# Performance work log

Measured on AMD Instinct MI355X. Metric: run time of the kernel, lower is better.

## Reference

```python
import jax, jax.numpy as jnp
import numpy as np

N = 100000
E = 1600000
IN_CH = 32
HID = 64
HEADS = 2
NUM_CLASSES = 12
NEG_SLOPE = 0.2


def gat_conv(x, src, dst, W, a_src, a_dst, bias, concat):
    """PyG-style GATConv (self-loops already appended to src/dst).
    x: [N, F_in], W: [F_in, H*C], a_src/a_dst: [H, C], bias: [H*C] or [C]."""
    n = x.shape[0]
    h = (x @ W).reshape(n, HEADS, -1)                    # [N, H, C]
    al_s = jnp.einsum('nhc,hc->nh', h, a_src)            # [N, H]
    al_d = jnp.einsum('nhc,hc->nh', h, a_dst)            # [N, H]
    e = jax.nn.leaky_relu(al_s[src] + al_d[dst], NEG_SLOPE)  # [Etot, H]
    # segment softmax over destination neighborhoods
    e_max = jax.ops.segment_max(e, dst, num_segments=n)      # [N, H]
    ex = jnp.exp(e - e_max[dst])                              # [Etot, H]
    denom = jax.ops.segment_sum(ex, dst, num_segments=n)     # [N, H]
    alpha = ex / denom[dst]                                   # [Etot, H]
    msg = h[src] * alpha[:, :, None]                          # [Etot, H, C]
    out = jax.ops.segment_sum(msg, dst, num_segments=n)      # [N, H, C]
    if concat:
        out = out.reshape(n, -1)
    else:
        out = out.mean(axis=1)
    return out + bias


def prelu(x, a):
    return jnp.where(x >= 0, x, a * x)


def setup_inputs() -> dict:
    key = jax.random.key(0)
    ks = jax.random.split(key, 16)
    HC = HEADS * HID
    d = {
        'x': jax.random.normal(ks[0], (N, IN_CH), jnp.float32),
        'edge_index': jax.random.randint(ks[1], (2, E), 0, N, jnp.int32),
        'W1': jax.random.normal(ks[2], (IN_CH, HC), jnp.float32) * 0.1,
        'a1s': jax.random.normal(ks[3], (HEADS, HID), jnp.float32) * 0.1,
        'a1d': jax.random.normal(ks[4], (HEADS, HID), jnp.float32) * 0.1,
        'b1': jnp.zeros((HC,), jnp.float32),
        'W2': jax.random.normal(ks[5], (HC, HC), jnp.float32) * 0.1,
        'a2s': jax.random.normal(ks[6], (HEADS, HID), jnp.float32) * 0.1,
        'a2d': jax.random.normal(ks[7], (HEADS, HID), jnp.float32) * 0.1,
        'b2': jnp.zeros((HC,), jnp.float32),
        'W3': jax.random.normal(ks[8], (HC, HC), jnp.float32) * 0.1,
        'a3s': jax.random.normal(ks[9], (HEADS, HID), jnp.float32) * 0.1,
        'a3d': jax.random.normal(ks[10], (HEADS, HID), jnp.float32) * 0.1,
        'b3': jnp.zeros((HID,), jnp.float32),
        'prelu_a': jnp.float32(0.25),
        'Wc': jax.random.normal(ks[11], (HID, NUM_CLASSES), jnp.float32) * 0.1,
        'bc': jnp.zeros((NUM_CLASSES,), jnp.float32),
    }
    return d


def reference(x, edge_index, W1, a1s, a1d, b1, W2, a2s, a2d, b2,
              W3, a3s, a3d, b3, prelu_a, Wc, bc):
    loops = jnp.arange(N, dtype=edge_index.dtype)
    src = jnp.concatenate([edge_index[0], loops])
    dst = jnp.concatenate([edge_index[1], loops])
    h = gat_conv(x, src, dst, W1, a1s, a1d, b1, concat=True)
    h = prelu(h, prelu_a)
    h = gat_conv(h, src, dst, W2, a2s, a2d, b2, concat=True)
    h = prelu(h, prelu_a)
    h = gat_conv(h, src, dst, W3, a3s, a3d, b3, concat=False)
    h = prelu(h, prelu_a)
    return h @ Wc + bc
```

## Files before the change

### kernel.cpp

```cpp
#include <hip/hip_runtime.h>
#include <stdint.h>

#define NN 100000
#define NE 1600000
#define ET (NE + NN)
#define HC 128
#define HID 64
#define NCLS 12
#define BSZ 512
#define NBK ((NN + BSZ - 1) / BSZ)
#define CHUNK 8192
#define NPB ((ET + CHUNK - 1) / CHUNK)

typedef _Float16 f16;
typedef _Float16 f16x2 __attribute__((ext_vector_type(2)));
typedef _Float16 f16x4 __attribute__((ext_vector_type(4)));
typedef _Float16 f16x8 __attribute__((ext_vector_type(8)));

__global__ void k_init(int* bucketTotal) {
    int i = threadIdx.x;
    if (i < NBK) bucketTotal[i] = 0;
}

__global__ __launch_bounds__(256) void k_hist(const int* __restrict__ ei, int* __restrict__ bucketTotal) {
    __shared__ int h[NBK];
    int tid = threadIdx.x;
    for (int b = tid; b < NBK; b += 256) h[b] = 0;
    __syncthreads();
    long base = (long)blockIdx.x * CHUNK;
#pragma unroll
    for (int k = 0; k < CHUNK / 256; k++) {
        long i = base + k * 256 + tid;
        if (i < ET) {
            int d = (i < NE) ? ei[NE + i] : (int)(i - NE);
            atomicAdd(&h[d >> 9], 1);
        }
    }
    __syncthreads();
    for (int b = tid; b < NBK; b += 256)
        if (h[b]) atomicAdd(&bucketTotal[b], h[b]);
}

__global__ __launch_bounds__(256) void k_bscan(const int* __restrict__ bucketTotal,
                                               int* __restrict__ bucketStart,
                                               int* __restrict__ bucketFill,
                                               int* __restrict__ rp) {
    __shared__ int s[256];
    int tid = threadIdx.x;
    int v = (tid < NBK) ? bucketTotal[tid] : 0;
    s[tid] = v;
    __syncthreads();
    for (int o = 1; o < 256; o <<= 1) {
        int t = (tid >= o) ? s[tid - o] : 0;
        __syncthreads();
        s[tid] += t;
        __syncthreads();
    }
    if (tid < NBK) {
        int excl = s[tid] - v;
        bucketStart[tid] = excl;
        bucketFill[tid] = excl;
    }
    if (tid == 0) { bucketStart[NBK] = ET; rp[NN] = ET; }
}

__global__ __launch_bounds__(256) void k_part(const int* __restrict__ ei,
                                              int* __restrict__ bucketFill,
                                              uint32_t* __restrict__ ebuf) {
    __shared__ int h[NBK];
    __shared__ int base[NBK];
    int tid = threadIdx.x;
    for (int b = tid; b < NBK; b += 256) h[b] = 0;
    __syncthreads();
    long cbase = (long)blockIdx.x * CHUNK;
#pragma unroll
    for (int k = 0; k < CHUNK / 256; k++) {
        long i = cbase + k * 256 + tid;
        if (i < ET) {
            int d = (i < NE) ? ei[NE + i] : (int)(i - NE);
            atomicAdd(&h[d >> 9], 1);
        }
    }
    __syncthreads();
    for (int b = tid; b < NBK; b += 256)
        base[b] = h[b] ? atomicAdd(&bucketFill[b], h[b]) : 0;
    __syncthreads();
    for (int b = tid; b < NBK; b += 256) h[b] = 0;
    __syncthreads();
#pragma unroll
    for (int k = 0; k < CHUNK / 256; k++) {
        long i = cbase + k * 256 + tid;
        if (i < ET) {
            int s, d;
            if (i < NE) { s = ei[i]; d = ei[NE + i]; } else { s = d = (int)(i - NE); }
            int bk = d >> 9;
            int off = atomicAdd(&h[bk], 1);
            ebuf[base[bk] + off] = (uint32_t)s | ((uint32_t)(d & 511) << 17);
        }
    }
}

__global__ __launch_bounds__(512) void k_build(const uint32_t* __restrict__ ebuf,
                                               const int* __restrict__ bucketStart,
                                               int* __restrict__ rp, int* __restrict__ colx) {
    __shared__ int cnt[BSZ];
    __shared__ int fill[BSZ];
    int b = blockIdx.x, tid = threadIdx.x;
    int e0 = bucketStart[b], e1 = bucketStart[b + 1], m = e1 - e0;
    cnt[tid] = 0;
    __syncthreads();
    for (int k = tid; k < m; k += 512) atomicAdd(&cnt[ebuf[e0 + k] >> 17], 1);
    __syncthreads();
    int v = cnt[tid];
    __syncthreads();
    cnt[tid] = v;
    __syncthreads();
    for (int o = 1; o < 512; o <<= 1) {
        int t = (tid >= o) ? cnt[tid - o] : 0;
        __syncthreads();
        cnt[tid] += t;
        __syncthreads();
    }
    int excl = cnt[tid] - v;
    int node = b * BSZ + tid;
    if (node < NN) rp[node] = e0 + excl;
    fill[tid] = e0 + excl;
    __syncthreads();
    for (int k = tid; k < m; k += 512) {
        uint32_t e = ebuf[e0 + k];
        int pos = atomicAdd(&fill[e >> 17], 1);
        colx[pos] = (int)(e & 0x1FFFF);
    }
}

__global__ __launch_bounds__(256) void k_att1(const float* __restrict__ x,
                                              const float* __restrict__ W1,
                                              const float* __restrict__ a1s,
                                              const float* __restrict__ a1d,
                                              f16* __restrict__ x16,
                                              float* __restrict__ als, float* __restrict__ ald) {
    __shared__ float sIn[128 * 33];
    __shared__ float spv[128];
    int t = threadIdx.x;
    long n0 = (long)blockIdx.x * 128;
    if (t < 128) {
        int sd = t >> 6, h = (t >> 5) & 1, f = t & 31;
        const float* a = sd ? a1d : a1s;
        float acc = 0.f;
        for (int c = 0; c < 64; c++) acc = fmaf(W1[f * HC + h * 64 + c], a[h * 64 + c], acc);
        spv[t] = acc;
    }
    for (int c = t; c < 128 * 8; c += 256) {
        int row = c >> 3, col = (c & 7) * 4;
        long gn = n0 + row;
        if (gn < NN) {
            float4 v = *(const float4*)(x + gn * 32 + col);
            float* dst = &sIn[row * 33 + col];
            dst[0] = v.x; dst[1] = v.y; dst[2] = v.z; dst[3] = v.w;
            f16x4 o;
            o[0] = (f16)v.x; o[1] = (f16)v.y; o[2] = (f16)v.z; o[3] = (f16)v.w;
            *(f16x4*)(x16 + gn * 32 + col) = o;
        }
    }
    __syncthreads();
    int n = t >> 1, h = t & 1;
    long gn = n0 + n;
    if (gn >= NN) return;
    const float* row = &sIn[n * 33];
    const float* as_ = &spv[h * 32];
    const float* ad_ = &spv[64 + h * 32];
    float s_ = 0.f, d_ = 0.f;
#pragma unroll
    for (int f = 0; f < 32; f++) {
        float v = row[f];
        s_ = fmaf(v, as_[f], s_);
        d_ = fmaf(v, ad_[f], d_);
    }
    als[2 * gn + h] = s_;
    ald[2 * gn + h] = d_;
}

__global__ __launch_bounds__(256) void k_aggx(const int* __restrict__ rp, const int* __restrict__ colx,
                                              const f16* __restrict__ x16,
                                              const float* __restrict__ als, const float* __restrict__ ald,
                                              float* __restrict__ xbar) {
    int wid = blockIdx.x * 4 + (threadIdx.x >> 6);
    int lane = threadIdx.x & 63;
    int g = lane >> 2, li = lane & 3;
    int start = rp[wid], end = rp[wid + 1];
    float2 adv = *(const float2*)(ald + 2 * wid);
    float a0[8], a1[8];
#pragma unroll
    for (int k = 0; k < 8; k++) { a0[k] = 0.f; a1[k] = 0.f; }
    float ws0 = 0.f, ws1 = 0.f;
#pragma unroll 2
    for (int j0 = start; j0 < end; j0 += 16) {
        int j = j0 + g;
        int jc = j < end ? j : end - 1;
        int s = colx[jc];
        float2 asv = *(const float2*)(als + 2 * s);
        float e0 = asv.x + adv.x, e1 = asv.y + adv.y;
        e0 = fmaxf(e0, 0.2f * e0);
        e1 = fmaxf(e1, 0.2f * e1);
        float w0 = __expf(e0), w1 = __expf(e1);
        if (j >= end) { w0 = 0.f; w1 = 0.f; }
        ws0 += w0; ws1 += w1;
        f16x8 xv = *(const f16x8*)(x16 + (long)s * 32 + li * 8);
#pragma unroll
        for (int k = 0; k < 8; k++) {
            float f = (float)xv[k];
            a0[k] = fmaf(w0, f, a0[k]);
            a1[k] = fmaf(w1, f, a1[k]);
        }
    }
#pragma unroll
    for (int o = 4; o <= 32; o <<= 1) {
        ws0 += __shfl_xor(ws0, o);
        ws1 += __shfl_xor(ws1, o);
#pragma unroll
        for (int k = 0; k < 8; k++) {
            a0[k] += __shfl_xor(a0[k], o);
            a1[k] += __shfl_xor(a1[k], o);
        }
    }
    float inv0 = 1.0f / ws0, inv1 = 1.0f / ws1;
    int head = g >> 3, q = g & 7;
    float val = head ? a1[q] * inv1 : a0[q] * inv0;
    xbar[(long)wid * 64 + head * 32 + li * 8 + q] = val;
}

__global__ __launch_bounds__(256) void k_post1(const float* __restrict__ xb,
                                               const float* __restrict__ W1,
                                               const float* __restrict__ b1,
                                               const float* __restrict__ pap,
                                               float* __restrict__ outp) {
    __shared__ __align__(16) float sIn[64 * 64];
    __shared__ __align__(16) float sW[32 * HC];
    __shared__ float sB[HC];
    int tid = threadIdx.x;
    long n0 = (long)blockIdx.x * 64;
    for (int c = tid; c < 64 * 16; c += 256) {
        int row = c >> 4, col = (c & 15) * 4;
        long gn = n0 + row;
        float4 v = make_float4(0.f, 0.f, 0.f, 0.f);
        if (gn < NN) v = *(const float4*)(xb + gn * 64 + col);
        *(float4*)(sIn + row * 64 + col) = v;
    }
    for (int c = tid; c < 32 * HC / 4; c += 256) ((float4*)sW)[c] = ((const float4*)W1)[c];
    if (tid < HC) sB[tid] = b1[tid];
    __syncthreads();
    int cg = tid & 31, ng = tid >> 5, head = cg >> 4;
    float4 acc[8];
#pragma unroll
    for (int i = 0; i < 8; i++) acc[i] = make_float4(0.f, 0.f, 0.f, 0.f);
    for (int k = 0; k < 32; k++) {
        float4 w = *(const float4*)(sW + k * HC + cg * 4);
#pragma unroll
        for (int i = 0; i < 8; i++) {
            float a = sIn[(ng * 8 + i) * 64 + head * 32 + k];
            acc[i].x = fmaf(a, w.x, acc[i].x);
            acc[i].y = fmaf(a, w.y, acc[i].y);
            acc[i].z = fmaf(a, w.z, acc[i].z);
            acc[i].w = fmaf(a, w.w, acc[i].w);
        }
    }
    float pa = pap[0];
    float4 b = *(const float4*)(sB + cg * 4);
#pragma unroll
    for (int i = 0; i < 8; i++) {
        long n = n0 + ng * 8 + i;
        if (n < NN) {
            float4 o;
            o.x = acc[i].x + b.x; o.y = acc[i].y + b.y;
            o.z = acc[i].z + b.z; o.w = acc[i].w + b.w;
            o.x = o.x >= 0.f ? o.x : pa * o.x;
            o.y = o.y >= 0.f ? o.y : pa * o.y;
            o.z = o.z >= 0.f ? o.z : pa * o.z;
            o.w = o.w >= 0.f ? o.w : pa * o.w;
            *(float4*)(outp + n * HC + cg * 4) = o;
        }
    }
}

__global__ __launch_bounds__(256) void k_gemm(const float* __restrict__ xg,
                                              const float* __restrict__ Wg,
                                              const float* __restrict__ avs,
                                              const float* __restrict__ avd,
                                              f16* __restrict__ h16,
                                              float* __restrict__ als, float* __restrict__ ald) {
    constexpr int K = 128, KT = 64;
    __shared__ __align__(16) float sIn[64 * KT];
    __shared__ __align__(16) float sW[KT * HC];
    __shared__ float sas[HC], sad[HC];
    int tid = threadIdx.x;
    long n0 = (long)blockIdx.x * 64;
    if (tid < HC) { sas[tid] = avs[tid]; sad[tid] = avd[tid]; }
    int cg = tid & 31, ng = tid >> 5;
    float4 acc[8];
#pragma unroll
    for (int i = 0; i < 8; i++) acc[i] = make_float4(0.f, 0.f, 0.f, 0.f);

    for (int kt = 0; kt < K; kt += KT) {
        __syncthreads();
        const float4* wsrc = (const float4*)(Wg + (long)kt * HC);
        for (int c = tid; c < KT * HC / 4; c += 256) ((float4*)sW)[c] = wsrc[c];
        for (int c = tid; c < 64 * KT / 4; c += 256) {
            int row = c / (KT / 4), kc = c % (KT / 4);
            long gn = n0 + row;
            float4 v = make_float4(0.f, 0.f, 0.f, 0.f);
            if (gn < NN) v = *(const float4*)(xg + gn * K + kt + kc * 4);
            *(float4*)(sIn + row * KT + kc * 4) = v;
        }
        __syncthreads();
        for (int k = 0; k < KT; k += 4) {
            float4 w0 = *(const float4*)(sW + (k + 0) * HC + cg * 4);
            float4 w1 = *(const float4*)(sW + (k + 1) * HC + cg * 4);
            float4 w2 = *(const float4*)(sW + (k + 2) * HC + cg * 4);
            float4 w3 = *(const float4*)(sW + (k + 3) * HC + cg * 4);
#pragma unroll
            for (int i = 0; i < 8; i++) {
                float4 a = *(const float4*)(sIn + (ng * 8 + i) * KT + k);
                acc[i].x = fmaf(a.x, w0.x, acc[i].x); acc[i].y = fmaf(a.x, w0.y, acc[i].y);
                acc[i].z = fmaf(a.x, w0.z, acc[i].z); acc[i].w = fmaf(a.x, w0.w, acc[i].w);
                acc[i].x = fmaf(a.y, w1.x, acc[i].x); acc[i].y = fmaf(a.y, w1.y, acc[i].y);
                acc[i].z = fmaf(a.y, w1.z, acc[i].z); acc[i].w = fmaf(a.y, w1.w, acc[i].w);
                acc[i].x = fmaf(a.z, w2.x, acc[i].x); acc[i].y = fmaf(a.z, w2.y, acc[i].y);
                acc[i].z = fmaf(a.z, w2.z, acc[i].z); acc[i].w = fmaf(a.z, w2.w, acc[i].w);
                acc[i].x = fmaf(a.w, w3.x, acc[i].x); acc[i].y = fmaf(a.w, w3.y, acc[i].y);
                acc[i].z = fmaf(a.w, w3.z, acc[i].z); acc[i].w = fmaf(a.w, w3.w, acc[i].w);
            }
        }
    }
    int head = cg >> 4;
#pragma unroll
    for (int i = 0; i < 8; i++) {
        long n = n0 + ng * 8 + i;
        if (n < NN) {
            f16x4 o;
            o[0] = (f16)acc[i].x; o[1] = (f16)acc[i].y;
            o[2] = (f16)acc[i].z; o[3] = (f16)acc[i].w;
            *(f16x4*)(h16 + n * HC + cg * 4) = o;
        }
        const float* ap = (const float*)&acc[i];
        float s_ = 0.f, d_ = 0.f;
#pragma unroll
        for (int j = 0; j < 4; j++) {
            int c = cg * 4 + j;
            s_ = fmaf(ap[j], sas[c], s_);
            d_ = fmaf(ap[j], sad[c], d_);
        }
#pragma unroll
        for (int o = 8; o; o >>= 1) { s_ += __shfl_xor(s_, o); d_ += __shfl_xor(d_, o); }
        if ((cg & 15) == 0 && n < NN) {
            als[2 * n + head] = s_;
            ald[2 * n + head] = d_;
        }
    }
}

template <int MEAN>
__global__ __launch_bounds__(256) void k_agg(const int* __restrict__ rp, const int* __restrict__ colx,
                                             const f16* __restrict__ h,
                                             const float* __restrict__ als, const float* __restrict__ ald,
                                             const float* __restrict__ bias,
                                             const float* __restrict__ pap,
                                             float* __restrict__ outp) {
    int wid = blockIdx.x * 4 + (threadIdx.x >> 6);
    int lane = threadIdx.x & 63;
    int g = lane >> 4, li = lane & 15;
    int start = rp[wid], end = rp[wid + 1];
    float2 adv = *(const float2*)(ald + 2 * wid);
    float acc[8];
#pragma unroll
    for (int k = 0; k < 8; k++) acc[k] = 0.f;
    float ws0 = 0.f, ws1 = 0.f;
    bool head1 = li >= 8;
#pragma unroll 4
    for (int j0 = start; j0 < end; j0 += 4) {
        int j = j0 + g;
        int jc = j < end ? j : end - 1;
        int s = colx[jc];
        float2 asv = *(const float2*)(als + 2 * s);
        float e0 = asv.x + adv.x, e1 = asv.y + adv.y;
        e0 = fmaxf(e0, 0.2f * e0);
        e1 = fmaxf(e1, 0.2f * e1);
        float w0 = __expf(e0), w1 = __expf(e1);
        if (j >= end) { w0 = 0.f; w1 = 0.f; }
        ws0 += w0; ws1 += w1;
        f16x8 hv = *(const f16x8*)(h + (long)s * HC + li * 8);
        float wsel = head1 ? w1 : w0;
#pragma unroll
        for (int k = 0; k < 8; k++) acc[k] = fmaf(wsel, (float)hv[k], acc[k]);
    }
#pragma unroll
    for (int o = 16; o <= 32; o <<= 1) {
        ws0 += __shfl_xor(ws0, o);
        ws1 += __shfl_xor(ws1, o);
#pragma unroll
        for (int k = 0; k < 8; k++) acc[k] += __shfl_xor(acc[k], o);
    }
    float pa = pap[0];
    if (!MEAN) {
        float inv = 1.0f / (head1 ? ws1 : ws0);
        int c = li * 8 + g * 2;
        float2 bu = *(const float2*)(bias + c);
        float o0 = acc[g * 2] * inv + bu.x;
        float o1 = acc[g * 2 + 1] * inv + bu.y;
        o0 = o0 >= 0.f ? o0 : pa * o0;
        o1 = o1 >= 0.f ? o1 : pa * o1;
        *(float2*)(outp + (long)wid * HC + c) = make_float2(o0, o1);
    } else {
        float inv = 1.0f / (head1 ? ws1 : ws0);
        float v0 = acc[g * 2] * inv, v1 = acc[g * 2 + 1] * inv;
        float p0 = __shfl_xor(v0, 8), p1 = __shfl_xor(v1, 8);
        if (!head1) {
            int c = li * 8 + g * 2;
            float2 bu = *(const float2*)(bias + c);
            float o0 = 0.5f * (v0 + p0) + bu.x;
            float o1 = 0.5f * (v1 + p1) + bu.y;
            o0 = o0 >= 0.f ? o0 : pa * o0;
            o1 = o1 >= 0.f ? o1 : pa * o1;
            *(float2*)(outp + (long)wid * HID + c) = make_float2(o0, o1);
        }
    }
}

__global__ __launch_bounds__(256) void k_cls(const float* __restrict__ hin,
                                             const float* __restrict__ Wc,
                                             const float* __restrict__ bcp,
                                             float* __restrict__ outp) {
    __shared__ float sW[HID * NCLS];
    __shared__ float sb[NCLS];
    int tid = threadIdx.x;
    for (int c = tid; c < HID * NCLS; c += 256) sW[c] = Wc[c];
    if (tid < NCLS) sb[tid] = bcp[tid];
    __syncthreads();
    int n = blockIdx.x * 256 + tid;
    if (n >= NN) return;
    float o[NCLS];
#pragma unroll
    for (int k = 0; k < NCLS; k++) o[k] = sb[k];
    const float* row = hin + (long)n * HID;
#pragma unroll 8
    for (int c = 0; c < HID; c++) {
        float v = row[c];
#pragma unroll
        for (int k = 0; k < NCLS; k++) o[k] = fmaf(v, sW[c * NCLS + k], o[k]);
    }
#pragma unroll
    for (int k = 0; k < NCLS; k += 2)
        *(float2*)(outp + (long)n * NCLS + k) = make_float2(o[k], o[k + 1]);
}

extern "C" void kernel_launch(void* const* d_in, const int* in_sizes, int n_in,
                              void* d_out, int out_size, void* d_ws, size_t ws_size,
                              hipStream_t stream) {
    const float* x   = (const float*)d_in[0];
    const int*   ei  = (const int*)d_in[1];
    const float* W1  = (const float*)d_in[2];
    const float* a1s = (const float*)d_in[3];
    const float* a1d = (const float*)d_in[4];
    const float* b1  = (const float*)d_in[5];
    const float* W2  = (const float*)d_in[6];
    const float* a2s = (const float*)d_in[7];
    const float* a2d = (const float*)d_in[8];
    const float* b2  = (const float*)d_in[9];
    const float* W3  = (const float*)d_in[10];
    const float* a3s = (const float*)d_in[11];
    const float* a3d = (const float*)d_in[12];
    const float* b3  = (const float*)d_in[13];
    const float* pa  = (const float*)d_in[14];
    const float* Wc  = (const float*)d_in[15];
    const float* bc  = (const float*)d_in[16];
    float* out = (float*)d_out;

    char* w = (char*)d_ws;
    size_t off = 0;
    auto take = [&](size_t b) { void* p = w + off; off += (b + 255) & ~(size_t)255; return p; };
    int* rp      = (int*)take((size_t)(NN + 1) * 4);
    int* colx    = (int*)take((size_t)ET * 4);
    int* btot    = (int*)take((size_t)NBK * 4);
    int* bstart  = (int*)take((size_t)(NBK + 1) * 4);
    int* bfill   = (int*)take((size_t)NBK * 4);
    float* als   = (float*)take((size_t)NN * 8);
    float* ald   = (float*)take((size_t)NN * 8);
    f16* x16     = (f16*)take((size_t)NN * 32 * 2);
    f16* h16     = (f16*)take((size_t)NN * HC * 2);
    float* xbar  = (float*)take((size_t)NN * 64 * 4);
    float* bufB  = (float*)take((size_t)NN * HC * 4);
    uint32_t* ebuf = (uint32_t*)h16;

    int nb = (NN + 255) / 256;
    int gb = (NN + 63) / 64;
    int ab = NN / 4;
    int tb = (NN + 127) / 128;

    k_init<<<1, 256, 0, stream>>>(btot);
    k_hist<<<NPB, 256, 0, stream>>>(ei, btot);
    k_bscan<<<1, 256, 0, stream>>>(btot, bstart, bfill, rp);
    k_part<<<NPB, 256, 0, stream>>>(ei, bfill, ebuf);
    k_build<<<NBK, 512, 0, stream>>>(ebuf, bstart, rp, colx);

    k_att1<<<tb, 256, 0, stream>>>(x, W1, a1s, a1d, x16, als, ald);
    k_aggx<<<ab, 256, 0, stream>>>(rp, colx, x16, als, ald, xbar);
    k_post1<<<gb, 256, 0, stream>>>(xbar, W1, b1, pa, bufB);
    k_gemm<<<gb, 256, 0, stream>>>(bufB, W2, a2s, a2d, h16, als, ald);
    k_agg<0><<<ab, 256, 0, stream>>>(rp, colx, h16, als, ald, b2, pa, bufB);
    k_gemm<<<gb, 256, 0, stream>>>(bufB, W3, a3s, a3d, h16, als, ald);
    k_agg<1><<<ab, 256, 0, stream>>>(rp, colx, h16, als, ald, b3, pa, bufB);
    k_cls<<<nb, 256, 0, stream>>>(bufB, Wc, bc, out);
}
```

Before: 524.1 us.

## Use MFMA fp16 GEMM with hi/lo split weights and fp16 intermediate activations

Replaces the fp32 FMA GEMMs for layers 2 and 3 with MFMA 16x16x32 fp16 instructions. The weights are pre-split into hi and lo fp16 fragments to keep accuracy, and a new kernel lays them out in MFMA fragment order. Post-layer activations are now stored in fp16 instead of fp32, which halves GEMM input traffic, and the aggx kernel is reworked to use 16 lanes per feature with 4 edges in flight. This risks some precision loss, since the activations are rounded to fp16.

```diff
diff --git a/kernel.cpp b/kernel.cpp
--- a/kernel.cpp
+++ b/kernel.cpp
@@ -16,6 +16,7 @@
 typedef _Float16 f16x2 __attribute__((ext_vector_type(2)));
 typedef _Float16 f16x4 __attribute__((ext_vector_type(4)));
 typedef _Float16 f16x8 __attribute__((ext_vector_type(8)));
+typedef float f32x4 __attribute__((ext_vector_type(4)));
 
 __global__ void k_init(int* bucketTotal) {
     int i = threadIdx.x;
@@ -130,6 +131,27 @@
         uint32_t e = ebuf[e0 + k];
         int pos = atomicAdd(&fill[e >> 17], 1);
         colx[pos] = (int)(e & 0x1FFFF);
+    }
+}
+
+__global__ void k_wt(const float* __restrict__ W2, const float* __restrict__ W3,
+                     f16* __restrict__ wout) {
+    const float* W = blockIdx.x ? W3 : W2;
+    f16* hi = wout + (size_t)blockIdx.x * 2 * 2048 * 8;
+    f16* lo = hi + 2048 * 8;
+    for (int s = threadIdx.x; s < 2048; s += 256) {
+        int kk = s >> 9, nt = (s >> 6) & 7, l = s & 63;
+        int n = nt * 16 + (l & 15), k0 = kk * 32 + (l >> 4) * 8;
+        f16x8 vh, vl;
+#pragma unroll
+        for (int j = 0; j < 8; j++) {
+            float v = W[(long)(k0 + j) * HC + n];
+            f16 h = (f16)v;
+            vh[j] = h;
+            vl[j] = (f16)(v - (float)h);
+        }
+        *(f16x8*)(hi + (size_t)s * 8) = vh;
+        *(f16x8*)(lo + (size_t)s * 8) = vl;
     }
 }
 
@@ -186,15 +208,12 @@
                                               float* __restrict__ xbar) {
     int wid = blockIdx.x * 4 + (threadIdx.x >> 6);
     int lane = threadIdx.x & 63;
-    int g = lane >> 2, li = lane & 3;
+    int g = lane >> 4, li = lane & 15;
     int start = rp[wid], end = rp[wid + 1];
     float2 adv = *(const float2*)(ald + 2 * wid);
-    float a0[8], a1[8];
-#pragma unroll
-    for (int k = 0; k < 8; k++) { a0[k] = 0.f; a1[k] = 0.f; }
-    float ws0 = 0.f, ws1 = 0.f;
-#pragma unroll 2
-    for (int j0 = start; j0 < end; j0 += 16) {
+    float a00 = 0.f, a01 = 0.f, a10 = 0.f, a11 = 0.f, ws0 = 0.f, ws1 = 0.f;
+#pragma unroll 4
+    for (int j0 = start; j0 < end; j0 += 4) {
         int j = j0 + g;
         int jc = j < end ? j : end - 1;
         int s = colx[jc];
@@ -205,35 +224,31 @@
         float w0 = __expf(e0), w1 = __expf(e1);
         if (j >= end) { w0 = 0.f; w1 = 0.f; }
         ws0 += w0; ws1 += w1;
-        f16x8 xv = *(const f16x8*)(x16 + (long)s * 32 + li * 8);
-#pragma unroll
-        for (int k = 0; k < 8; k++) {
-            float f = (float)xv[k];
-            a0[k] = fmaf(w0, f, a0[k]);
-            a1[k] = fmaf(w1, f, a1[k]);
-        }
-    }
-#pragma unroll
-    for (int o = 4; o <= 32; o <<= 1) {
-        ws0 += __shfl_xor(ws0, o);
-        ws1 += __shfl_xor(ws1, o);
-#pragma unroll
-        for (int k = 0; k < 8; k++) {
-            a0[k] += __shfl_xor(a0[k], o);
-            a1[k] += __shfl_xor(a1[k], o);
-        }
-    }
-    float inv0 = 1.0f / ws0, inv1 = 1.0f / ws1;
-    int head = g >> 3, q = g & 7;
-    float val = head ? a1[q] * inv1 : a0[q] * inv0;
-    xbar[(long)wid * 64 + head * 32 + li * 8 + q] = val;
+        f16x2 xv = *(const f16x2*)(x16 + (long)s * 32 + li * 2);
+        float f0 = (float)xv[0], f1 = (float)xv[1];
+        a00 = fmaf(w0, f0, a00); a01 = fmaf(w0, f1, a01);
+        a10 = fmaf(w1, f0, a10); a11 = fmaf(w1, f1, a11);
+    }
+#pragma unroll
+    for (int o = 16; o <= 32; o <<= 1) {
+        ws0 += __shfl_xor(ws0, o); ws1 += __shfl_xor(ws1, o);
+        a00 += __shfl_xor(a00, o); a01 += __shfl_xor(a01, o);
+        a10 += __shfl_xor(a10, o); a11 += __shfl_xor(a11, o);
+    }
+    if (g == 0) {
+        float inv = 1.0f / ws0;
+        *(float2*)(xbar + (long)wid * 64 + li * 2) = make_float2(a00 * inv, a01 * inv);
+    } else if (g == 1) {
+        float inv = 1.0f / ws1;
+        *(float2*)(xbar + (long)wid * 64 + 32 + li * 2) = make_float2(a10 * inv, a11 * inv);
+    }
 }
 
 __global__ __launch_bounds__(256) void k_post1(const float* __restrict__ xb,
                                                const float* __restrict__ W1,
                                                const float* __restrict__ b1,
                                                const float* __restrict__ pap,
-                                               float* __restrict__ outp) {
+                                               f16* __restrict__ outp) {
     __shared__ __align__(16) float sIn[64 * 64];
     __shared__ __align__(16) float sW[32 * HC];
     __shared__ float sB[HC];
@@ -270,90 +285,76 @@
     for (int i = 0; i < 8; i++) {
         long n = n0 + ng * 8 + i;
         if (n < NN) {
-            float4 o;
-            o.x = acc[i].x + b.x; o.y = acc[i].y + b.y;
-            o.z = acc[i].z + b.z; o.w = acc[i].w + b.w;
-            o.x = o.x >= 0.f ? o.x : pa * o.x;
-            o.y = o.y >= 0.f ? o.y : pa * o.y;
-            o.z = o.z >= 0.f ? o.z : pa * o.z;
-            o.w = o.w >= 0.f ? o.w : pa * o.w;
-            *(float4*)(outp + n * HC + cg * 4) = o;
-        }
-    }
-}
-
-__global__ __launch_bounds__(256) void k_gemm(const float* __restrict__ xg,
-                                              const float* __restrict__ Wg,
-                                              const float* __restrict__ avs,
-                                              const float* __restrict__ avd,
-                                              f16* __restrict__ h16,
-                                              float* __restrict__ als, float* __restrict__ ald) {
-    constexpr int K = 128, KT = 64;
-    __shared__ __align__(16) float sIn[64 * KT];
-    __shared__ __align__(16) float sW[KT * HC];
-    __shared__ float sas[HC], sad[HC];
+            float o0 = acc[i].x + b.x, o1 = acc[i].y + b.y;
+            float o2 = acc[i].z + b.z, o3 = acc[i].w + b.w;
+            o0 = o0 >= 0.f ? o0 : pa * o0;
+            o1 = o1 >= 0.f ? o1 : pa * o1;
+            o2 = o2 >= 0.f ? o2 : pa * o2;
+            o3 = o3 >= 0.f ? o3 : pa * o3;
+            f16x4 o; o[0] = (f16)o0; o[1] = (f16)o1; o[2] = (f16)o2; o[3] = (f16)o3;
+            *(f16x4*)(outp + n * HC + cg * 4) = o;
+        }
+    }
+}
+
+__global__ __launch_bounds__(256) void k_gemmM(const f16* __restrict__ in16,
+                                               const f16* __restrict__ wfrag,
+                                               const float* __restrict__ avs,
+                                               const float* __restrict__ avd,
+                                               f16* __restrict__ h16,
+                                               float* __restrict__ als, float* __restrict__ ald) {
+    const f16* whi = wfrag;
+    const f16* wlo = wfrag + 2048 * 8;
     int tid = threadIdx.x;
+    int w = tid >> 6, l = tid & 63, q = l >> 4, m = l & 15;
     long n0 = (long)blockIdx.x * 64;
-    if (tid < HC) { sas[tid] = avs[tid]; sad[tid] = avd[tid]; }
-    int cg = tid & 31, ng = tid >> 5;
-    float4 acc[8];
-#pragma unroll
-    for (int i = 0; i < 8; i++) acc[i] = make_float4(0.f, 0.f, 0.f, 0.f);
-
-    for (int kt = 0; kt < K; kt += KT) {
-        __syncthreads();
-        const float4* wsrc = (const float4*)(Wg + (long)kt * HC);
-        for (int c = tid; c < KT * HC / 4; c += 256) ((float4*)sW)[c] = wsrc[c];
-        for (int c = tid; c < 64 * KT / 4; c += 256) {
-            int row = c / (KT / 4), kc = c % (KT / 4);
-            long gn = n0 + row;
-            float4 v = make_float4(0.f, 0.f, 0.f, 0.f);
-            if (gn < NN) v = *(const float4*)(xg + gn * K + kt + kc * 4);
-            *(float4*)(sIn + row * KT + kc * 4) = v;
-        }
-        __syncthreads();
-        for (int k = 0; k < KT; k += 4) {
-            float4 w0 = *(const float4*)(sW + (k + 0) * HC + cg * 4);
-            float4 w1 = *(const float4*)(sW + (k + 1) * HC + cg * 4);
-            float4 w2 = *(const float4*)(sW + (k + 2) * HC + cg * 4);
-            float4 w3 = *(const float4*)(sW + (k + 3) * HC + cg * 4);
-#pragma unroll
-            for (int i = 0; i < 8; i++) {
-                float4 a = *(const float4*)(sIn + (ng * 8 + i) * KT + k);
-                acc[i].x = fmaf(a.x, w0.x, acc[i].x); acc[i].y = fmaf(a.x, w0.y, acc[i].y);
-                acc[i].z = fmaf(a.x, w0.z, acc[i].z); acc[i].w = fmaf(a.x, w0.w, acc[i].w);
-                acc[i].x = fmaf(a.y, w1.x, acc[i].x); acc[i].y = fmaf(a.y, w1.y, acc[i].y);
-                acc[i].z = fmaf(a.y, w1.z, acc[i].z); acc[i].w = fmaf(a.y, w1.w, acc[i].w);
-                acc[i].x = fmaf(a.z, w2.x, acc[i].x); acc[i].y = fmaf(a.z, w2.y, acc[i].y);
-                acc[i].z = fmaf(a.z, w2.z, acc[i].z); acc[i].w = fmaf(a.z, w2.w, acc[i].w);
-                acc[i].x = fmaf(a.w, w3.x, acc[i].x); acc[i].y = fmaf(a.w, w3.y, acc[i].y);
-                acc[i].z = fmaf(a.w, w3.z, acc[i].z); acc[i].w = fmaf(a.w, w3.w, acc[i].w);
-            }
-        }
-    }
-    int head = cg >> 4;
-#pragma unroll
-    for (int i = 0; i < 8; i++) {
-        long n = n0 + ng * 8 + i;
-        if (n < NN) {
-            f16x4 o;
-            o[0] = (f16)acc[i].x; o[1] = (f16)acc[i].y;
-            o[2] = (f16)acc[i].z; o[3] = (f16)acc[i].w;
-            *(f16x4*)(h16 + n * HC + cg * 4) = o;
-        }
-        const float* ap = (const float*)&acc[i];
-        float s_ = 0.f, d_ = 0.f;
-#pragma unroll
-        for (int j = 0; j < 4; j++) {
-            int c = cg * 4 + j;
-            s_ = fmaf(ap[j], sas[c], s_);
-            d_ = fmaf(ap[j], sad[c], d_);
-        }
-#pragma unroll
-        for (int o = 8; o; o >>= 1) { s_ += __shfl_xor(s_, o); d_ += __shfl_xor(d_, o); }
-        if ((cg & 15) == 0 && n < NN) {
-            als[2 * n + head] = s_;
-            ald[2 * n + head] = d_;
+    long rowg = n0 + w * 16 + m;
+    bool rok = rowg < NN;
+    f32x4 acc[8];
+#pragma unroll
+    for (int i = 0; i < 8; i++) acc[i] = (f32x4){0.f, 0.f, 0.f, 0.f};
+#pragma unroll
+    for (int kk = 0; kk < 4; kk++) {
+        f16x8 a = {};
+        if (rok) a = *(const f16x8*)(in16 + rowg * HC + kk * 32 + q * 8);
+#pragma unroll
+        for (int nt = 0; nt < 8; nt++) {
+            f16x8 bh = *(const f16x8*)(whi + ((kk * 8 + nt) * 64 + l) * 8);
+            f16x8 bl = *(const f16x8*)(wlo + ((kk * 8 + nt) * 64 + l) * 8);
+            acc[nt] = __builtin_amdgcn_mfma_f32_16x16x32_f16(a, bh, acc[nt], 0, 0, 0);
+            acc[nt] = __builtin_amdgcn_mfma_f32_16x16x32_f16(a, bl, acc[nt], 0, 0, 0);
+        }
+    }
+    float as_[8], ad_[8];
+#pragma unroll
+    for (int nt = 0; nt < 8; nt++) { as_[nt] = avs[nt * 16 + m]; ad_[nt] = avd[nt * 16 + m]; }
+#pragma unroll
+    for (int r = 0; r < 4; r++) {
+        long rg = n0 + w * 16 + q * 4 + r;
+        bool ok = rg < NN;
+        float s0 = 0.f, s1 = 0.f, d0 = 0.f, d1 = 0.f;
+#pragma unroll
+        for (int nt = 0; nt < 4; nt++) {
+            float v = acc[nt][r];
+            s0 = fmaf(v, as_[nt], s0); d0 = fmaf(v, ad_[nt], d0);
+        }
+#pragma unroll
+        for (int nt = 4; nt < 8; nt++) {
+            float v = acc[nt][r];
+            s1 = fmaf(v, as_[nt], s1); d1 = fmaf(v, ad_[nt], d1);
+        }
+        if (ok) {
+#pragma unroll
+            for (int nt = 0; nt < 8; nt++) h16[rg * HC + nt * 16 + m] = (f16)acc[nt][r];
+        }
+#pragma unroll
+        for (int o = 1; o <= 8; o <<= 1) {
+            s0 += __shfl_xor(s0, o); s1 += __shfl_xor(s1, o);
+            d0 += __shfl_xor(d0, o); d1 += __shfl_xor(d1, o);
+        }
+        if (ok && m == 0) {
+            als[2 * rg] = s0; als[2 * rg + 1] = s1;
+            ald[2 * rg] = d0; ald[2 * rg + 1] = d1;
         }
     }
 }
@@ -364,7 +365,8 @@
                                              const float* __restrict__ als, const float* __restrict__ ald,
                                              const float* __restrict__ bias,
                                              const float* __restrict__ pap,
-                                             float* __restrict__ outp) {
+                                             f16* __restrict__ out16,
+                                             float* __restrict__ outf) {
     int wid = blockIdx.x * 4 + (threadIdx.x >> 6);
     int lane = threadIdx.x & 63;
     int g = lane >> 4, li = lane & 15;
@@ -408,7 +410,8 @@
         float o1 = acc[g * 2 + 1] * inv + bu.y;
         o0 = o0 >= 0.f ? o0 : pa * o0;
         o1 = o1 >= 0.f ? o1 : pa * o1;
-        *(float2*)(outp + (long)wid * HC + c) = make_float2(o0, o1);
+        f16x2 o; o[0] = (f16)o0; o[1] = (f16)o1;
+        *(f16x2*)(out16 + (long)wid * HC + c) = o;
     } else {
         float inv = 1.0f / (head1 ? ws1 : ws0);
         float v0 = acc[g * 2] * inv, v1 = acc[g * 2 + 1] * inv;
@@ -420,7 +423,7 @@
             float o1 = 0.5f * (v1 + p1) + bu.y;
             o0 = o0 >= 0.f ? o0 : pa * o0;
             o1 = o1 >= 0.f ? o1 : pa * o1;
-            *(float2*)(outp + (long)wid * HID + c) = make_float2(o0, o1);
+            *(float2*)(outf + (long)wid * HID + c) = make_float2(o0, o1);
         }
     }
 }
@@ -484,10 +487,12 @@
     int* bfill   = (int*)take((size_t)NBK * 4);
     float* als   = (float*)take((size_t)NN * 8);
     float* ald   = (float*)take((size_t)NN * 8);
+    f16* wfrag   = (f16*)take((size_t)2 * 2 * 2048 * 8 * 2);
     f16* x16     = (f16*)take((size_t)NN * 32 * 2);
     f16* h16     = (f16*)take((size_t)NN * HC * 2);
+    f16* g16     = (f16*)take((size_t)NN * HC * 2);
     float* xbar  = (float*)take((size_t)NN * 64 * 4);
-    float* bufB  = (float*)take((size_t)NN * HC * 4);
+    float* bufB  = (float*)take((size_t)NN * HID * 4);
     uint32_t* ebuf = (uint32_t*)h16;
 
     int nb = (NN + 255) / 256;
@@ -500,13 +505,14 @@
     k_bscan<<<1, 256, 0, stream>>>(btot, bstart, bfill, rp);
     k_part<<<NPB, 256, 0, stream>>>(ei, bfill, ebuf);
     k_build<<<NBK, 512, 0, stream>>>(ebuf, bstart, rp, colx);
+    k_wt<<<2, 256, 0, stream>>>(W2, W3, wfrag);
 
     k_att1<<<tb, 256, 0, stream>>>(x, W1, a1s, a1d, x16, als, ald);
     k_aggx<<<ab, 256, 0, stream>>>(rp, colx, x16, als, ald, xbar);
-    k_post1<<<gb, 256, 0, stream>>>(xbar, W1, b1, pa, bufB);
-    k_gemm<<<gb, 256, 0, stream>>>(bufB, W2, a2s, a2d, h16, als, ald);
-    k_agg<0><<<ab, 256, 0, stream>>>(rp, colx, h16, als, ald, b2, pa, bufB);
-    k_gemm<<<gb, 256, 0, stream>>>(bufB, W3, a3s, a3d, h16, als, ald);
-    k_agg<1><<<ab, 256, 0, stream>>>(rp, colx, h16, als, ald, b3, pa, bufB);
+    k_post1<<<gb, 256, 0, stream>>>(xbar, W1, b1, pa, g16);
+    k_gemmM<<<gb, 256, 0, stream>>>(g16, wfrag, a2s, a2d, h16, als, ald);
+    k_agg<0><<<ab, 256, 0, stream>>>(rp, colx, h16, als, ald, b2, pa, g16, nullptr);
+    k_gemmM<<<gb, 256, 0, stream>>>(g16, wfrag + (size_t)2 * 2048 * 8, a3s, a3d, h16, als, ald);
+    k_agg<1><<<ab, 256, 0, stream>>>(rp, colx, h16, als, ald, b3, pa, nullptr, bufB);
     k_cls<<<nb, 256, 0, stream>>>(bufB, Wc, bc, out);
 }
```

Measured after the change: 442.1 us. -15.6%, faster.
